# Kernel tuning notes

Measured on AMD Instinct MI355X. Metric: run time of the kernel, lower is better.

The kernel has to match this reference:

```python
import jax, jax.numpy as jnp
import numpy as np

N_NODES = 50000
N_EDGES = 800000
VOCAB = 4096          # node_emb_size
EMB_DIM = 128         # node_emb_dim
HIDDEN = 128          # hidden_dim -> layer1 out = 2*HIDDEN
N_POS = 1024


def gcn_conv(h, edge_index, W, b, n):
    """PyG GCNConv: lin -> add self loops -> sym-normalized scatter-add -> +bias."""
    h = h @ W                                   # [N, out]
    row, col = edge_index[0], edge_index[1]     # source, target
    loop = jnp.arange(n)
    row = jnp.concatenate([row, loop])
    col = jnp.concatenate([col, loop])
    deg = jax.ops.segment_sum(jnp.ones(row.shape[0], dtype=h.dtype), col, num_segments=n)
    dinv = jnp.where(deg > 0, jax.lax.rsqrt(deg), 0.0)
    norm = dinv[row] * dinv[col]                # [E+N]
    msg = h[row] * norm[:, None]                # gather + scale
    return jax.ops.segment_sum(msg, col, num_segments=n) + b


def setup_inputs() -> dict:
    key = jax.random.key(0)
    ks = jax.random.split(key, 10)
    x = jax.random.randint(ks[0], (N_NODES, 1), 0, VOCAB)
    edge_index = jax.random.randint(ks[1], (2, N_EDGES), 0, N_NODES)
    x_position = jax.random.randint(ks[2], (N_POS,), 0, N_NODES)
    # Embedding init: normal(0, emb_dim^-0.5) per initialize_parameters
    emb = jax.random.normal(ks[3], (VOCAB, EMB_DIM), jnp.float32) * EMB_DIM ** -0.5
    # GCN / linear weights (glorot-ish)
    W1 = jax.random.normal(ks[4], (EMB_DIM, 2 * HIDDEN), jnp.float32) * (EMB_DIM ** -0.5)
    b1 = jnp.zeros((2 * HIDDEN,), jnp.float32)
    W2 = jax.random.normal(ks[5], (2 * HIDDEN, HIDDEN), jnp.float32) * ((2 * HIDDEN) ** -0.5)
    b2 = jnp.zeros((HIDDEN,), jnp.float32)
    Wc = jax.random.normal(ks[6], (HIDDEN, VOCAB), jnp.float32) * (HIDDEN ** -0.5)
    bc = jnp.zeros((VOCAB,), jnp.float32)
    return {"x": x, "edge_index": edge_index, "x_position": x_position,
            "emb": emb, "W1": W1, "b1": b1, "W2": W2, "b2": b2, "Wc": Wc, "bc": bc}


def reference(x, edge_index, x_position, emb, W1, b1, W2, b2, Wc, bc):
    n = x.shape[0]
    h = emb[x[:, 0]]                                   # Embedding + squeeze(1)
    h = jax.nn.relu(gcn_conv(h, edge_index, W1, b1, n))
    z = gcn_conv(h, edge_index, W2, b2, n)             # [N, HIDDEN]
    logits = z @ Wc + bc                               # classifier over all nodes
    # embedding stage: mean of classified rows at x_position, keep dim 0
    return jnp.mean(logits[x_position], axis=0, keepdims=True)  # [1, VOCAB]
```

## Files before the change

### kernel.cpp

```cpp
#include <hip/hip_runtime.h>

constexpr int EMB  = 128;
constexpr int H1D  = 256;
constexpr int H2D  = 128;
constexpr int VOC  = 4096;
constexpr int NSL  = 32;

__global__ void k_init(int* cnt, int* count, unsigned int* flagbits, unsigned int* markw,
                       float* wagg, float* wsum, int* nflag, int* total,
                       int n, int nwords) {
    int i = blockIdx.x * blockDim.x + threadIdx.x;
    if (i < n) { cnt[i] = 0; count[i] = 0; wagg[i] = 0.0f; }
    if (i < nwords) { flagbits[i] = 0u; markw[i] = 0u; }
    if (i < NSL * H1D) wsum[i] = 0.0f;
    if (i == 0) { *nflag = 0; *total = 0; }
}

constexpr int RPB = 16;
__global__ void k_embW1C(const float* __restrict__ emb, const float* __restrict__ W1,
                         float* __restrict__ embW1,
                         const int* __restrict__ xpos, int* count,
                         unsigned int* flagbits, int np) {
    int t = threadIdx.x;
    if (blockIdx.x == VOC / RPB) {
        for (int p = t; p < np; p += blockDim.x) {
            int v = xpos[p];
            atomicAdd(&count[v], 1);
            atomicOr(&flagbits[v >> 5], 1u << (v & 31));
        }
        return;
    }
    __shared__ float er[RPB][EMB];
    int r0 = blockIdx.x * RPB;
    for (int i = t; i < RPB * EMB; i += 256) {
        er[i / EMB][i % EMB] = emb[(size_t)r0 * EMB + i];
    }
    __syncthreads();
    float acc[RPB];
#pragma unroll
    for (int rr = 0; rr < RPB; rr++) acc[rr] = 0.0f;
    for (int k = 0; k < EMB; k++) {
        float w = W1[k * H1D + t];
#pragma unroll
        for (int rr = 0; rr < RPB; rr++) acc[rr] += er[rr][k] * w;
    }
#pragma unroll
    for (int rr = 0; rr < RPB; rr++) {
        embW1[(size_t)(r0 + rr) * H1D + t] = acc[rr];
    }
}

__global__ void k_hist(const int* __restrict__ row, const int* __restrict__ col,
                       const unsigned int* __restrict__ flagbits, int* cnt,
                       unsigned int* markw, int ne) {
    int e = blockIdx.x * blockDim.x + threadIdx.x;
    if (e < ne) {
        int c = col[e];
        atomicAdd(&cnt[c], 1);
        if ((flagbits[c >> 5] >> (c & 31)) & 1u) {
            int r = row[e];
            atomicOr(&markw[r >> 5], 1u << (r & 31));
        }
    }
}

__global__ void k_alloc(unsigned int* needw,
                        const unsigned int* __restrict__ flagbits,
                        const int* __restrict__ cnt, const int* __restrict__ count,
                        float* wagg, int* needlist, int* nflag, int* total,
                        int* offs, int* cursor, int n) {
    int v = blockIdx.x * blockDim.x + threadIdx.x;
    int lane = threadIdx.x & 63;
    int cv = 0;
    bool need = false;
    if (v < n) {
        cv = cnt[v];
        bool mark = (needw[v >> 5] >> (v & 31)) & 1u;
        bool flag = (flagbits[v >> 5] >> (v & 31)) & 1u;
        need = mark || flag;
        if (flag) wagg[v] = (float)count[v] / ((float)cv + 1.0f);
    }
    unsigned long long nm = __ballot(need);
    int wbase = (v & ~63) >> 5;
    if (lane == 0)  needw[wbase]     = (unsigned int)(nm & 0xffffffffu);
    if (lane == 32) needw[wbase + 1] = (unsigned int)(nm >> 32);
    int seg = need ? cv : 0;
    int incl = seg;
#pragma unroll
    for (int d = 1; d < 64; d <<= 1) {
        int t = __shfl_up(incl, d);
        if (lane >= d) incl += t;
    }
    int excl = incl - seg;
    int wave_total = __shfl(incl, 63);
    int rank = __popcll(nm & ((1ull << lane) - 1));
    int wcnt = __popcll(nm);
    int base_id = 0, base_off = 0;
    if (lane == 0) {
        if (wcnt > 0) base_id = atomicAdd(nflag, wcnt);
        if (wave_total > 0) base_off = atomicAdd(total, wave_total);
    }
    base_id  = __shfl(base_id, 0);
    base_off = __shfl(base_off, 0);
    if (need) {
        needlist[base_id + rank] = v;
        int o = base_off + excl;
        offs[v] = o;
        cursor[v] = o;
    }
}

__global__ void k_scatter(const int* __restrict__ row, const int* __restrict__ col,
                          const unsigned int* __restrict__ needw,
                          const unsigned int* __restrict__ flagbits,
                          const int* __restrict__ count,
                          const int* __restrict__ x, const int* __restrict__ cnt,
                          int* cursor, int2* srowp, float* wagg, int ne) {
    int e = blockIdx.x * blockDim.x + threadIdx.x;
    if (e < ne) {
        int c = col[e];
        if ((needw[c >> 5] >> (c & 31)) & 1u) {
            int r = row[e];
            int pos = atomicAdd(&cursor[c], 1);
            float dr = rsqrtf((float)cnt[r] + 1.0f);
            int2 pk; pk.x = x[r]; pk.y = __float_as_int(dr);
            srowp[pos] = pk;
            if ((flagbits[c >> 5] >> (c & 31)) & 1u) {
                float dc = rsqrtf((float)cnt[c] + 1.0f);
                atomicAdd(&wagg[r], (float)count[c] * dc * dr);
            }
        }
    }
}

__global__ void k_fconv(const int* __restrict__ needlist, const int* __restrict__ nneed_p,
                        const float* __restrict__ wagg, const int* __restrict__ x,
                        const int2* __restrict__ srowp,
                        const int* __restrict__ offs, const int* __restrict__ cnt,
                        const float* __restrict__ embW1, const float* __restrict__ b1,
                        float* __restrict__ wsum) {
    int lane = threadIdx.x & 63;
    int wib  = threadIdx.x >> 6;
    int wid  = blockIdx.x * (blockDim.x >> 6) + wib;
    int nw   = gridDim.x * (blockDim.x >> 6);
    int nn   = *nneed_p;
    const float4* __restrict__ ew = (const float4*)embW1;
    float4 bfrag = ((const float4*)b1)[lane];
    float4 acc2 = {0.0f, 0.0f, 0.0f, 0.0f};

    for (int i = wid; i < nn; i += nw) {
        int v = needlist[i];
        int cv = cnt[v];
        float dv = rsqrtf((float)cv + 1.0f);
        float wa = wagg[v];
        float4 s = ew[(size_t)x[v] * 64 + lane];
        float w0 = dv * dv;
        float4 acc;
        acc.x = bfrag.x + w0 * s.x;
        acc.y = bfrag.y + w0 * s.y;
        acc.z = bfrag.z + w0 * s.z;
        acc.w = bfrag.w + w0 * s.w;
        int start = offs[v], m = cv;
        for (int base = 0; base < m; base += 64) {
            int mm = min(64, m - base);
            int xr = 0; float wr = 0.0f;
            if (lane < mm) {
                int2 pk = srowp[start + base + lane];
                xr = pk.x;
                wr = __int_as_float(pk.y) * dv;
            }
            int e = 0;
            for (; e + 4 <= mm; e += 4) {
                int i0 = __shfl(xr, e),     i1 = __shfl(xr, e + 1);
                int i2 = __shfl(xr, e + 2), i3 = __shfl(xr, e + 3);
                float q0 = __shfl(wr, e),     q1 = __shfl(wr, e + 1);
                float q2 = __shfl(wr, e + 2), q3 = __shfl(wr, e + 3);
                float4 t0 = ew[(size_t)i0 * 64 + lane];
                float4 t1 = ew[(size_t)i1 * 64 + lane];
                float4 t2 = ew[(size_t)i2 * 64 + lane];
                float4 t3 = ew[(size_t)i3 * 64 + lane];
                acc.x += q0 * t0.x + q1 * t1.x + q2 * t2.x + q3 * t3.x;
                acc.y += q0 * t0.y + q1 * t1.y + q2 * t2.y + q3 * t3.y;
                acc.z += q0 * t0.z + q1 * t1.z + q2 * t2.z + q3 * t3.z;
                acc.w += q0 * t0.w + q1 * t1.w + q2 * t2.w + q3 * t3.w;
            }
            for (; e < mm; e++) {
                int i0 = __shfl(xr, e);
                float q0 = __shfl(wr, e);
                float4 t0 = ew[(size_t)i0 * 64 + lane];
                acc.x += q0 * t0.x;
                acc.y += q0 * t0.y;
                acc.z += q0 * t0.z;
                acc.w += q0 * t0.w;
            }
        }
        acc2.x += wa * fmaxf(acc.x, 0.0f);
        acc2.y += wa * fmaxf(acc.y, 0.0f);
        acc2.z += wa * fmaxf(acc.z, 0.0f);
        acc2.w += wa * fmaxf(acc.w, 0.0f);
    }

    __shared__ float red[4][H1D];
    red[wib][4 * lane + 0] = acc2.x;
    red[wib][4 * lane + 1] = acc2.y;
    red[wib][4 * lane + 2] = acc2.z;
    red[wib][4 * lane + 3] = acc2.w;
    __syncthreads();
    int t = threadIdx.x;
    float ssum = red[0][t] + red[1][t] + red[2][t] + red[3][t];
    atomicAdd(&wsum[(blockIdx.x & (NSL - 1)) * H1D + t], ssum);
}

__global__ void k_zout(const float* __restrict__ wsum, const float* __restrict__ W2,
                       const float* __restrict__ b2, const float* __restrict__ Wc,
                       const float* __restrict__ bc, float* __restrict__ out,
                       float inv_np) {
    __shared__ float ws[H1D];
    __shared__ float z[H2D];
    int t = threadIdx.x;
    float s = 0.0f;
#pragma unroll
    for (int c = 0; c < NSL; c++) s += wsum[c * H1D + t];
    ws[t] = s;
    __syncthreads();
    if (t < H2D) {
        float acc = 0.0f;
#pragma unroll 8
        for (int k = 0; k < H1D; k++) acc += ws[k] * W2[k * H2D + t];
        z[t] = b2[t] + acc * inv_np;
    }
    __syncthreads();
    int c = blockIdx.x * blockDim.x + t;
    float acc = bc[c];
#pragma unroll 8
    for (int j = 0; j < H2D; j++) acc += z[j] * Wc[(size_t)j * VOC + c];
    out[c] = acc;
}

extern "C" void kernel_launch(void* const* d_in, const int* in_sizes, int n_in,
                              void* d_out, int out_size, void* d_ws, size_t ws_size,
                              hipStream_t stream) {
    const int n  = in_sizes[0];
    const int ne = in_sizes[1] / 2;
    const int np = in_sizes[2];

    const int*   x    = (const int*)d_in[0];
    const int*   ei   = (const int*)d_in[1];
    const int*   xpos = (const int*)d_in[2];
    const float* emb  = (const float*)d_in[3];
    const float* W1   = (const float*)d_in[4];
    const float* b1   = (const float*)d_in[5];
    const float* W2   = (const float*)d_in[6];
    const float* b2   = (const float*)d_in[7];
    const float* Wc   = (const float*)d_in[8];
    const float* bc   = (const float*)d_in[9];
    float*       out  = (float*)d_out;

    const int* row = ei;
    const int* col = ei + ne;

    char* p = (char*)d_ws;
    auto alloc = [&](size_t bytes) {
        char* r = p;
        p += (bytes + 255) & ~(size_t)255;
        return r;
    };
    const int nb     = (n + 255) / 256;
    const int neb    = (ne + 255) / 256;
    const int nwords = nb * 8;

    int*          cnt      = (int*)alloc((size_t)n * 4);
    int*          offs     = (int*)alloc((size_t)n * 4);
    int*          cursor   = (int*)alloc((size_t)n * 4);
    int*          count    = (int*)alloc((size_t)n * 4);
    int*          needlist = (int*)alloc((size_t)n * 4);
    unsigned int* needw    = (unsigned int*)alloc((size_t)nwords * 4);
    unsigned int* flagbits = (unsigned int*)alloc((size_t)nwords * 4);
    int2*         srowp    = (int2*)alloc((size_t)ne * 8);
    int*          nflag    = (int*)alloc(256 * 4);
    int*          total    = (int*)alloc(256 * 4);
    float*        wagg     = (float*)alloc((size_t)n * 4);
    float*        embW1    = (float*)alloc((size_t)VOC * H1D * 4);
    float*        wsum     = (float*)alloc((size_t)NSL * H1D * 4);

    k_init<<<nb, 256, 0, stream>>>(cnt, count, flagbits, needw, wagg, wsum,
                                   nflag, total, n, nwords);
    k_embW1C<<<VOC / RPB + 1, 256, 0, stream>>>(emb, W1, embW1, xpos, count, flagbits, np);
    k_hist<<<neb, 256, 0, stream>>>(row, col, flagbits, cnt, needw, ne);
    k_alloc<<<nb, 256, 0, stream>>>(needw, flagbits, cnt, count, wagg,
                                    needlist, nflag, total, offs, cursor, n);
    k_scatter<<<neb, 256, 0, stream>>>(row, col, needw, flagbits, count, x, cnt,
                                       cursor, srowp, wagg, ne);
    k_fconv<<<2048, 256, 0, stream>>>(needlist, nflag, wagg, x, srowp, offs, cnt,
                                      embW1, b1, wsum);
    k_zout<<<VOC / 256, 256, 0, stream>>>(wsum, W2, b2, Wc, bc, out, 1.0f / (float)np);
}
```

Measured before the change: 193.9 us.

## Fuse init with position flagging, GEMM with histogram, precompute node packs

Merges the init and position-flagging kernels, and runs the embedding×W1 GEMM concurrently with the edge-degree histogram in one launch. Precomputes a packed (x, inverse sqrt degree) array per node so the scatter does a single gather instead of two loads plus an rsqrt. The output projection kernel is split across more blocks with a 4-way K reduction for more parallelism. The merged init has block 0 zeroing the count and flag arrays serially, which may create a tail.

```diff
diff --git a/kernel.cpp b/kernel.cpp
--- a/kernel.cpp
+++ b/kernel.cpp
@@ -5,61 +5,67 @@
 constexpr int H2D  = 128;
 constexpr int VOC  = 4096;
 constexpr int NSL  = 32;
-
-__global__ void k_init(int* cnt, int* count, unsigned int* flagbits, unsigned int* markw,
-                       float* wagg, float* wsum, int* nflag, int* total,
-                       int n, int nwords) {
-    int i = blockIdx.x * blockDim.x + threadIdx.x;
-    if (i < n) { cnt[i] = 0; count[i] = 0; wagg[i] = 0.0f; }
-    if (i < nwords) { flagbits[i] = 0u; markw[i] = 0u; }
-    if (i < NSL * H1D) wsum[i] = 0.0f;
-    if (i == 0) { *nflag = 0; *total = 0; }
-}
-
-constexpr int RPB = 16;
-__global__ void k_embW1C(const float* __restrict__ emb, const float* __restrict__ W1,
-                         float* __restrict__ embW1,
-                         const int* __restrict__ xpos, int* count,
-                         unsigned int* flagbits, int np) {
+constexpr int RPB  = 16;
+
+__global__ void kA_init(int* cnt, int* count, unsigned int* flagbits, unsigned int* needw,
+                        float* wagg, float* wsum, int* nflag, int* total,
+                        const int* __restrict__ xpos,
+                        int n, int nwords, int np) {
     int t = threadIdx.x;
-    if (blockIdx.x == VOC / RPB) {
-        for (int p = t; p < np; p += blockDim.x) {
-            int v = xpos[p];
+    if (blockIdx.x == 0) {
+        for (int i = t; i < nwords; i += 256) flagbits[i] = 0u;
+        for (int i = t; i < n; i += 256) count[i] = 0;
+        __syncthreads();
+        for (int i = t; i < np; i += 256) {
+            int v = xpos[i];
             atomicAdd(&count[v], 1);
             atomicOr(&flagbits[v >> 5], 1u << (v & 31));
         }
-        return;
-    }
-    __shared__ float er[RPB][EMB];
-    int r0 = blockIdx.x * RPB;
-    for (int i = t; i < RPB * EMB; i += 256) {
-        er[i / EMB][i % EMB] = emb[(size_t)r0 * EMB + i];
-    }
-    __syncthreads();
-    float acc[RPB];
-#pragma unroll
-    for (int rr = 0; rr < RPB; rr++) acc[rr] = 0.0f;
-    for (int k = 0; k < EMB; k++) {
-        float w = W1[k * H1D + t];
-#pragma unroll
-        for (int rr = 0; rr < RPB; rr++) acc[rr] += er[rr][k] * w;
-    }
-#pragma unroll
-    for (int rr = 0; rr < RPB; rr++) {
-        embW1[(size_t)(r0 + rr) * H1D + t] = acc[rr];
-    }
-}
-
-__global__ void k_hist(const int* __restrict__ row, const int* __restrict__ col,
-                       const unsigned int* __restrict__ flagbits, int* cnt,
-                       unsigned int* markw, int ne) {
-    int e = blockIdx.x * blockDim.x + threadIdx.x;
-    if (e < ne) {
-        int c = col[e];
-        atomicAdd(&cnt[c], 1);
-        if ((flagbits[c >> 5] >> (c & 31)) & 1u) {
-            int r = row[e];
-            atomicOr(&markw[r >> 5], 1u << (r & 31));
+        if (t == 0) { *nflag = 0; *total = 0; }
+    } else {
+        const int stride = (gridDim.x - 1) * 256;
+        const int i0 = (blockIdx.x - 1) * 256 + t;
+        for (int i = i0; i < n; i += stride) { cnt[i] = 0; wagg[i] = 0.0f; }
+        for (int i = i0; i < nwords; i += stride) needw[i] = 0u;
+        for (int i = i0; i < NSL * H1D; i += stride) wsum[i] = 0.0f;
+    }
+}
+
+constexpr int KB_GRID = 1024;
+constexpr int GEMM_B  = 256;
+__global__ __launch_bounds__(256) void kB_embW1_hist(
+        const float* __restrict__ emb, const float* __restrict__ W1,
+        float* __restrict__ embW1,
+        const int* __restrict__ row, const int* __restrict__ col,
+        const unsigned int* __restrict__ flagbits,
+        int* cnt, unsigned int* markw, int ne) {
+    int t = threadIdx.x;
+    if (blockIdx.x < GEMM_B) {
+        __shared__ float er[RPB][EMB];
+        int r0 = blockIdx.x * RPB;
+        for (int i = t; i < RPB * EMB; i += 256)
+            er[i / EMB][i % EMB] = emb[(size_t)r0 * EMB + i];
+        __syncthreads();
+        float acc[RPB];
+#pragma unroll
+        for (int rr = 0; rr < RPB; rr++) acc[rr] = 0.0f;
+        for (int k = 0; k < EMB; k++) {
+            float w = W1[k * H1D + t];
+#pragma unroll
+            for (int rr = 0; rr < RPB; rr++) acc[rr] += er[rr][k] * w;
+        }
+#pragma unroll
+        for (int rr = 0; rr < RPB; rr++)
+            embW1[(size_t)(r0 + rr) * H1D + t] = acc[rr];
+    } else {
+        const int stride = (KB_GRID - GEMM_B) * 256;
+        for (int e = (blockIdx.x - GEMM_B) * 256 + t; e < ne; e += stride) {
+            int c = col[e];
+            atomicAdd(&cnt[c], 1);
+            if ((flagbits[c >> 5] >> (c & 31)) & 1u) {
+                int r = row[e];
+                atomicOr(&markw[r >> 5], 1u << (r & 31));
+            }
         }
     }
 }
@@ -67,14 +73,18 @@
 __global__ void k_alloc(unsigned int* needw,
                         const unsigned int* __restrict__ flagbits,
                         const int* __restrict__ cnt, const int* __restrict__ count,
+                        const int* __restrict__ x,
                         float* wagg, int* needlist, int* nflag, int* total,
-                        int* offs, int* cursor, int n) {
+                        int* offs, int* cursor, int2* pk, int n) {
     int v = blockIdx.x * blockDim.x + threadIdx.x;
     int lane = threadIdx.x & 63;
     int cv = 0;
     bool need = false;
     if (v < n) {
         cv = cnt[v];
+        float dv = rsqrtf((float)cv + 1.0f);
+        int2 p; p.x = x[v]; p.y = __float_as_int(dv);
+        pk[v] = p;
         bool mark = (needw[v >> 5] >> (v & 31)) & 1u;
         bool flag = (flagbits[v >> 5] >> (v & 31)) & 1u;
         need = mark || flag;
@@ -88,8 +98,8 @@
     int incl = seg;
 #pragma unroll
     for (int d = 1; d < 64; d <<= 1) {
-        int t = __shfl_up(incl, d);
-        if (lane >= d) incl += t;
+        int t2 = __shfl_up(incl, d);
+        if (lane >= d) incl += t2;
     }
     int excl = incl - seg;
     int wave_total = __shfl(incl, 63);
@@ -97,7 +107,7 @@
     int wcnt = __popcll(nm);
     int base_id = 0, base_off = 0;
     if (lane == 0) {
-        if (wcnt > 0) base_id = atomicAdd(nflag, wcnt);
+        if (wcnt > 0)       base_id  = atomicAdd(nflag, wcnt);
         if (wave_total > 0) base_off = atomicAdd(total, wave_total);
     }
     base_id  = __shfl(base_id, 0);
@@ -114,7 +124,7 @@
                           const unsigned int* __restrict__ needw,
                           const unsigned int* __restrict__ flagbits,
                           const int* __restrict__ count,
-                          const int* __restrict__ x, const int* __restrict__ cnt,
+                          const int2* __restrict__ pk,
                           int* cursor, int2* srowp, float* wagg, int ne) {
     int e = blockIdx.x * blockDim.x + threadIdx.x;
     if (e < ne) {
@@ -122,11 +132,11 @@
         if ((needw[c >> 5] >> (c & 31)) & 1u) {
             int r = row[e];
             int pos = atomicAdd(&cursor[c], 1);
-            float dr = rsqrtf((float)cnt[r] + 1.0f);
-            int2 pk; pk.x = x[r]; pk.y = __float_as_int(dr);
-            srowp[pos] = pk;
+            int2 pr = pk[r];
+            srowp[pos] = pr;
             if ((flagbits[c >> 5] >> (c & 31)) & 1u) {
-                float dc = rsqrtf((float)cnt[c] + 1.0f);
+                float dc = __int_as_float(pk[c].y);
+                float dr = __int_as_float(pr.y);
                 atomicAdd(&wagg[r], (float)count[c] * dc * dr);
             }
         }
@@ -165,9 +175,9 @@
             int mm = min(64, m - base);
             int xr = 0; float wr = 0.0f;
             if (lane < mm) {
-                int2 pk = srowp[start + base + lane];
-                xr = pk.x;
-                wr = __int_as_float(pk.y) * dv;
+                int2 pk2 = srowp[start + base + lane];
+                xr = pk2.x;
+                wr = __int_as_float(pk2.y) * dv;
             }
             int e = 0;
             for (; e + 4 <= mm; e += 4) {
@@ -217,10 +227,11 @@
                        float inv_np) {
     __shared__ float ws[H1D];
     __shared__ float z[H2D];
+    __shared__ float red[256];
     int t = threadIdx.x;
     float s = 0.0f;
 #pragma unroll
-    for (int c = 0; c < NSL; c++) s += wsum[c * H1D + t];
+    for (int c2 = 0; c2 < NSL; c2++) s += wsum[c2 * H1D + t];
     ws[t] = s;
     __syncthreads();
     if (t < H2D) {
@@ -230,11 +241,17 @@
         z[t] = b2[t] + acc * inv_np;
     }
     __syncthreads();
-    int c = blockIdx.x * blockDim.x + t;
-    float acc = bc[c];
+    int c  = blockIdx.x * 64 + (t & 63);
+    int ks = t >> 6;
+    float acc = 0.0f;
 #pragma unroll 8
-    for (int j = 0; j < H2D; j++) acc += z[j] * Wc[(size_t)j * VOC + c];
-    out[c] = acc;
+    for (int j = ks * 32; j < ks * 32 + 32; j++) acc += z[j] * Wc[(size_t)j * VOC + c];
+    red[t] = acc;
+    __syncthreads();
+    if (t < 64) {
+        int cc = blockIdx.x * 64 + t;
+        out[cc] = bc[cc] + red[t] + red[t + 64] + red[t + 128] + red[t + 192];
+    }
 }
 
 extern "C" void kernel_launch(void* const* d_in, const int* in_sizes, int n_in,
@@ -277,21 +294,22 @@
     unsigned int* needw    = (unsigned int*)alloc((size_t)nwords * 4);
     unsigned int* flagbits = (unsigned int*)alloc((size_t)nwords * 4);
     int2*         srowp    = (int2*)alloc((size_t)ne * 8);
+    int2*         pk       = (int2*)alloc((size_t)n * 8);
     int*          nflag    = (int*)alloc(256 * 4);
     int*          total    = (int*)alloc(256 * 4);
     float*        wagg     = (float*)alloc((size_t)n * 4);
     float*        embW1    = (float*)alloc((size_t)VOC * H1D * 4);
     float*        wsum     = (float*)alloc((size_t)NSL * H1D * 4);
 
-    k_init<<<nb, 256, 0, stream>>>(cnt, count, flagbits, needw, wagg, wsum,
-                                   nflag, total, n, nwords);
-    k_embW1C<<<VOC / RPB + 1, 256, 0, stream>>>(emb, W1, embW1, xpos, count, flagbits, np);
-    k_hist<<<neb, 256, 0, stream>>>(row, col, flagbits, cnt, needw, ne);
-    k_alloc<<<nb, 256, 0, stream>>>(needw, flagbits, cnt, count, wagg,
-                                    needlist, nflag, total, offs, cursor, n);
-    k_scatter<<<neb, 256, 0, stream>>>(row, col, needw, flagbits, count, x, cnt,
+    kA_init<<<nb, 256, 0, stream>>>(cnt, count, flagbits, needw, wagg, wsum,
+                                    nflag, total, xpos, n, nwords, np);
+    kB_embW1_hist<<<KB_GRID, 256, 0, stream>>>(emb, W1, embW1, row, col, flagbits,
+                                               cnt, needw, ne);
+    k_alloc<<<nb, 256, 0, stream>>>(needw, flagbits, cnt, count, x, wagg,
+                                    needlist, nflag, total, offs, cursor, pk, n);
+    k_scatter<<<neb, 256, 0, stream>>>(row, col, needw, flagbits, count, pk,
                                        cursor, srowp, wagg, ne);
     k_fconv<<<2048, 256, 0, stream>>>(needlist, nflag, wagg, x, srowp, offs, cnt,
                                       embW1, b1, wsum);
-    k_zout<<<VOC / 256, 256, 0, stream>>>(wsum, W2, b2, Wc, bc, out, 1.0f / (float)np);
-}
+    k_zout<<<VOC / 64, 256, 0, stream>>>(wsum, W2, b2, Wc, bc, out, 1.0f / (float)np);
+}
```

Measured after the change: 187.7 us. -3.2%, faster.
